# Optimization experiments

Measured on AMD Instinct MI355X. Metric: run time of the kernel, lower is better.

The kernel has to match this reference:

```python
import jax, jax.numpy as jnp
import numpy as np

HEADS = 8

def group_conv1x1(x, w, heads):
    # x: (B, Cin, H, W); w: (Cout, Cin//heads, 1, 1) grouped 1x1 conv, no bias
    B, Cin, H, W = x.shape
    Cout = w.shape[0]
    xg = x.reshape(B, heads, Cin // heads, H * W)
    wg = w[:, :, 0, 0].reshape(heads, Cout // heads, Cin // heads)
    out = jnp.einsum('hoc,bhcl->bhol', wg, xg)
    return out.reshape(B, Cout, H, W)

def sine_pe(d_model, length):
    # standard transformer sin/cos encoding, laid out as (d_model, length)
    pos = jnp.arange(length, dtype=jnp.float32)
    i = jnp.arange(0, d_model, 2, dtype=jnp.float32)
    div = jnp.exp(-(jnp.log(10000.0)) * i / d_model)
    ang = div[:, None] * pos[None, :]            # (d/2, L)
    pe = jnp.zeros((d_model, length), dtype=jnp.float32)
    pe = pe.at[0::2].set(jnp.sin(ang)).at[1::2].set(jnp.cos(ang))
    return pe

def setup_inputs() -> dict:
    key = jax.random.key(0)
    k0, k1, k2, k3 = jax.random.split(key, 4)
    B, Cin, H, W = 16, 256, 32, 32
    Cout, heads = 256, HEADS
    fan_out = Cout  # kaiming_normal fan_out for 1x1 conv = Cout*1*1
    std = np.sqrt(2.0 / fan_out)
    x = jax.random.normal(k0, (B, Cin, H, W), dtype=jnp.float32)
    wq = jax.random.normal(k1, (Cout, Cin // heads, 1, 1), dtype=jnp.float32) * std
    wk = jax.random.normal(k2, (Cout, Cin // heads, 1, 1), dtype=jnp.float32) * std
    wv = jax.random.normal(k3, (Cout, Cin // heads, 1, 1), dtype=jnp.float32) * std
    return {"x": x, "wq": wq, "wk": wk, "wv": wv}

def reference(x, wq, wk, wv):
    B, Cin, H, W = x.shape
    Cout = wq.shape[0]
    heads = HEADS
    dh = Cout // heads
    L = H * W

    q = group_conv1x1(x, wq, heads)              # (B, Cout, H, W)
    k = group_conv1x1(x, wk, heads)
    v = group_conv1x1(x, wv, heads)

    # sine positional encoding added to keys over flattened spatial positions
    k = k.reshape(B, Cout, L) + sine_pe(Cout, L)[None]

    q = q.reshape(B, heads, dh, L)               # (B, h, dh, L)
    k = k.reshape(B, heads, dh, L)
    v = v.reshape(B, heads, dh, L)

    scores = jnp.einsum('bhdq,bhdk->bhqk', q, k)  # (B, h, L, L) -- no sqrt(d) scaling, as in source
    attn = jax.nn.softmax(scores, axis=-1)
    out = jnp.einsum('bhqk,bhdk->bhdq', attn, v)  # (B, h, dh, L)
    return out.reshape(B, Cout, H, W)
```

## Files before the change

### kernel.cpp

```cpp
#include <hip/hip_runtime.h>

#define LL   1024
#define BHD  128
#define LOG2E 1.44269504088896340736f

typedef unsigned int       uint;
typedef unsigned short     ushort;
typedef unsigned long long ull;

typedef __attribute__((ext_vector_type(8)))  __bf16          bf16x8;
typedef __attribute__((ext_vector_type(8)))  unsigned short  u16x8;
typedef __attribute__((ext_vector_type(4)))  unsigned short  u16x4;
typedef __attribute__((ext_vector_type(4)))  uint            ui32x4;
typedef __attribute__((ext_vector_type(4)))  float           f32x4;
typedef __attribute__((ext_vector_type(16))) float           f32x16;

static __device__ __forceinline__ ushort f2bf(float f){
  union {float f; uint u;} v; v.f = f;
  uint u = v.u + 0x7fffu + ((v.u >> 16) & 1u);
  return (ushort)(u >> 16);
}
static __device__ __forceinline__ uint pack2(float a, float b){
  return (uint)f2bf(a) | ((uint)f2bf(b) << 16);
}
static __device__ __forceinline__ uint packtrunc(float a, float b){
  union {float f; uint u;} x, y; x.f = a; y.f = b;
  return __builtin_amdgcn_perm(y.u, x.u, 0x07060302u);
}
static __device__ __forceinline__ bf16x8 ld_frag(const ushort* p){
  u16x8 t = *(const u16x8*)p;
  return __builtin_bit_cast(bf16x8, t);
}
static __device__ __forceinline__ bf16x8 ld_frag64(const ushort* p){
  u16x4 a = *(const u16x4*)p;
  u16x4 b = *(const u16x4*)(p + 4);
  u16x8 t;
  t[0]=a[0]; t[1]=a[1]; t[2]=a[2]; t[3]=a[3];
  t[4]=b[0]; t[5]=b[1]; t[6]=b[2]; t[7]=b[3];
  return __builtin_bit_cast(bf16x8, t);
}

static __device__ __forceinline__ bool sniff_is_bf16(const uint* xw, int tid, int* cnt){
  uint w = xw[tid & 255];
  uint e = (w >> 7) & 0xFFu;
  bool hit = (e >= 118u) && (e <= 132u);
  ull b = __ballot(hit);
  if ((tid & 63) == 0) cnt[tid >> 6] = __popcll(b);
  __syncthreads();
  bool r = (cnt[0] + cnt[1] + cnt[2] + cnt[3]) > 128;
  __syncthreads();
  return r;
}

__global__ __launch_bounds__(256) void qkv_kernel(
    const void* __restrict__ xr,
    const void* __restrict__ wqr,
    const void* __restrict__ wkr,
    const void* __restrict__ wvr,
    ushort* __restrict__ Qt, ushort* __restrict__ Kt, ushort* __restrict__ Vt)
{
  const int bh   = blockIdx.x;
  const int lt   = blockIdx.y;
  const int tid  = threadIdx.x;
  const int wave = tid >> 6;
  const int lane = tid & 63;
  const int l16  = lane & 15;
  const int quad = lane >> 4;
  const int lbase = lt * 128;

  __shared__ int cnt[4];
  __shared__ __align__(16) uint xsd[128][20];

  const bool is_bf = sniff_is_bf16((const uint*)xr, tid, cnt);

  {
    const int cp = tid & 15, lg = tid >> 4;
    const size_t rb = (size_t)(bh*32 + 2*cp)*LL + lbase + lg*8;
    uint dw[8];
    if (is_bf){
      u16x8 e = *(const u16x8*)((const ushort*)xr + rb);
      u16x8 o = *(const u16x8*)((const ushort*)xr + rb + LL);
      #pragma unroll
      for (int j = 0; j < 8; ++j) dw[j] = (uint)e[j] | ((uint)o[j] << 16);
    } else {
      const float* xf = (const float*)xr;
      float4 e0 = *(const float4*)(xf + rb);
      float4 e1 = *(const float4*)(xf + rb + 4);
      float4 o0 = *(const float4*)(xf + rb + LL);
      float4 o1 = *(const float4*)(xf + rb + LL + 4);
      dw[0]=pack2(e0.x,o0.x); dw[1]=pack2(e0.y,o0.y);
      dw[2]=pack2(e0.z,o0.z); dw[3]=pack2(e0.w,o0.w);
      dw[4]=pack2(e1.x,o1.x); dw[5]=pack2(e1.y,o1.y);
      dw[6]=pack2(e1.z,o1.z); dw[7]=pack2(e1.w,o1.w);
    }
    #pragma unroll
    for (int j = 0; j < 8; ++j) xsd[lg*8 + j][cp] = dw[j];
  }
  __syncthreads();

  const void* wsrc[3] = {wqr, wkr, wvr};
  bf16x8 bw[3][2];
  #pragma unroll
  for (int p = 0; p < 3; ++p)
    #pragma unroll
    for (int nh = 0; nh < 2; ++nh){
      const int row = (bh & 7)*32 + nh*16 + l16;
      if (is_bf){
        bw[p][nh] = ld_frag((const ushort*)wsrc[p] + (size_t)row*32 + quad*8);
      } else {
        const float* wf = (const float*)wsrc[p] + (size_t)row*32 + quad*8;
        float4 f0 = *(const float4*)wf, f1 = *(const float4*)(wf + 4);
        u16x8 t;
        t[0]=f2bf(f0.x); t[1]=f2bf(f0.y); t[2]=f2bf(f0.z); t[3]=f2bf(f0.w);
        t[4]=f2bf(f1.x); t[5]=f2bf(f1.y); t[6]=f2bf(f1.z); t[7]=f2bf(f1.w);
        bw[p][nh] = __builtin_bit_cast(bf16x8, t);
      }
    }

  bf16x8 ax[2];
  #pragma unroll
  for (int mt = 0; mt < 2; ++mt)
    ax[mt] = __builtin_bit_cast(bf16x8,
               *(const ui32x4*)&xsd[wave*32 + mt*16 + l16][quad*4]);

  const f32x4 z = {0.f,0.f,0.f,0.f};
  f32x4 dq[2][2], dk[2][2], dv[2][2];
  #pragma unroll
  for (int mt = 0; mt < 2; ++mt)
    #pragma unroll
    for (int nh = 0; nh < 2; ++nh){
      dq[mt][nh] = __builtin_amdgcn_mfma_f32_16x16x32_bf16(ax[mt], bw[0][nh], z, 0,0,0);
      dk[mt][nh] = __builtin_amdgcn_mfma_f32_16x16x32_bf16(ax[mt], bw[1][nh], z, 0,0,0);
      dv[nh][mt] = __builtin_amdgcn_mfma_f32_16x16x32_bf16(bw[2][nh], ax[mt], z, 0,0,0);
    }

  #pragma unroll
  for (int mt = 0; mt < 2; ++mt)
    #pragma unroll
    for (int nh = 0; nh < 2; ++nh)
      #pragma unroll
      for (int r = 0; r < 4; ++r){
        const int l = lbase + wave*32 + mt*16 + quad*4 + r;
        const int d = nh*16 + l16;
        Qt[((size_t)bh*LL + l)*32 + d] = f2bf(dq[mt][nh][r]);
      }
  #pragma unroll
  for (int mt = 0; mt < 2; ++mt)
    #pragma unroll
    for (int nh = 0; nh < 2; ++nh){
      const int d = nh*16 + l16;
      const int c = (bh & 7)*32 + d;
      const float freq = __expf(-0.03597789207f * (float)(c & ~1));
      #pragma unroll
      for (int r = 0; r < 4; ++r){
        const int l = lbase + wave*32 + mt*16 + quad*4 + r;
        const float ang = freq * (float)l;
        const float pe  = (c & 1) ? __cosf(ang) : __sinf(ang);
        Kt[((size_t)bh*LL + l)*32 + d] = f2bf((dk[mt][nh][r] + pe) * LOG2E);
      }
    }
  #pragma unroll
  for (int dh = 0; dh < 2; ++dh)
    #pragma unroll
    for (int mt = 0; mt < 2; ++mt)
      #pragma unroll
      for (int r = 0; r < 4; ++r){
        const int d = dh*16 + quad*4 + r;
        const int l = lbase + wave*32 + mt*16 + l16;
        Vt[((size_t)(bh*32 + d))*LL + l] = f2bf(dv[dh][mt][r]);
      }
}

__global__ __launch_bounds__(256, 4) void attn_kernel(
    const void*   __restrict__ xr,
    const ushort* __restrict__ Qt,
    const ushort* __restrict__ Kt,
    const ushort* __restrict__ Vt,
    void* __restrict__ out)
{
  const int bh  = blockIdx.x;
  const int qt  = blockIdx.y;
  const int tid = threadIdx.x;
  const int wave = tid >> 6;
  const int lane = tid & 63;
  const int q32  = lane & 31;
  const int h    = lane >> 5;

  __shared__ int cnt[4];
  __shared__ __align__(16) ushort Ks[128][40];
  __shared__ __align__(16) ushort Vs[32][132];

  const bool is_bf = sniff_is_bf16((const uint*)xr, tid, cnt);

  const int qg = qt*128 + wave*32 + q32;
  const ushort* qrow = Qt + ((size_t)bh*LL + qg)*32;
  bf16x8 bq0 = ld_frag(qrow + h*8);
  bf16x8 bq1 = ld_frag(qrow + 16 + h*8);

  bf16x8 ones;
  { u16x8 t;
    #pragma unroll
    for (int j = 0; j < 8; ++j) t[j] = 0x3F80u;
    ones = __builtin_bit_cast(bf16x8, t); }

  const int skey = tid >> 1, shalf = tid & 1;
  const int rotw = (skey >> 2) & 3;
  const ushort* kg0 = Kt + ((size_t)(bh*LL + skey))*32 + (2*shalf)*8;
  ushort* kw0 = &Ks[skey][((2*shalf     + rotw) & 3)*8];
  ushort* kw1 = &Ks[skey][((2*shalf + 1 + rotw) & 3)*8];
  const int sd = tid >> 3, sg = tid & 7;
  const ushort* vgp = Vt + ((size_t)(bh*32 + sd))*LL + sg*16;
  ushort* vw = &Vs[sd][sg*16];

  const int rot = (q32 >> 2) & 3;
  const ushort* ka0 = &Ks[q32][((h + rot) & 3)*8];
  const ushort* ka1 = &Ks[q32][((2 + h + rot) & 3)*8];
  const ushort* vr  = &Vs[q32][h*8];

  f32x16 O = {};
  f32x16 R = {};

  u16x8 k0 = *(const u16x8*)kg0;
  u16x8 k1 = *(const u16x8*)(kg0 + 8);
  u16x8 v0 = *(const u16x8*)vgp;
  u16x8 v1 = *(const u16x8*)(vgp + 8);

  for (int it = 0; it < 8; ++it){
    __syncthreads();
    *(ui32x4*)kw0 = __builtin_bit_cast(ui32x4, k0);
    *(ui32x4*)kw1 = __builtin_bit_cast(ui32x4, k1);
    {
      u16x4 a, b;
      a[0]=v0[0]; a[1]=v0[1]; a[2]=v0[2]; a[3]=v0[3];
      b[0]=v0[4]; b[1]=v0[5]; b[2]=v0[6]; b[3]=v0[7];
      *(u16x4*)vw = a; *(u16x4*)(vw + 4) = b;
      a[0]=v1[0]; a[1]=v1[1]; a[2]=v1[2]; a[3]=v1[3];
      b[0]=v1[4]; b[1]=v1[5]; b[2]=v1[6]; b[3]=v1[7];
      *(u16x4*)(vw + 8) = a; *(u16x4*)(vw + 12) = b;
    }
    __syncthreads();
    if (it < 7){
      const int ko = (it + 1)*128;
      k0 = *(const u16x8*)(kg0 + (size_t)ko*32);
      k1 = *(const u16x8*)(kg0 + (size_t)ko*32 + 8);
      v0 = *(const u16x8*)(vgp + ko);
      v1 = *(const u16x8*)(vgp + ko + 8);
    }

    #pragma unroll
    for (int u = 0; u < 2; ++u){
      f32x16 st[2];
      #pragma unroll
      for (int tt = 0; tt < 2; ++tt){
        const int t = 2*u + tt;
        bf16x8 a0 = ld_frag(ka0 + t*32*40);
        bf16x8 a1 = ld_frag(ka1 + t*32*40);
        f32x16 zz = {};
        f32x16 s  = __builtin_amdgcn_mfma_f32_32x32x16_bf16(a0, bq0, zz, 0,0,0);
        st[tt]    = __builtin_amdgcn_mfma_f32_32x32x16_bf16(a1, bq1, s,  0,0,0);
      }

      uint pr[2][8];
      #pragma unroll
      for (int tt = 0; tt < 2; ++tt)
        #pragma unroll
        for (int zi = 0; zi < 8; ++zi){
          float p0 = __builtin_amdgcn_exp2f(st[tt][2*zi]);
          float p1 = __builtin_amdgcn_exp2f(st[tt][2*zi+1]);
          pr[tt][zi] = packtrunc(p0, p1);
        }

      #pragma unroll
      for (int c = 0; c < 4; ++c){
        const int tt = c >> 1, g0 = 4*(c & 1);
        uint s0 = h ? pr[tt][g0+0] : pr[tt][g0+2];
        uint s1 = h ? pr[tt][g0+1] : pr[tt][g0+3];
        uint r0 = (uint)__shfl_xor((int)s0, 32);
        uint r1 = (uint)__shfl_xor((int)s1, 32);
        ui32x4 pb;
        pb[0] = h ? r0 : pr[tt][g0+0];
        pb[1] = h ? r1 : pr[tt][g0+1];
        pb[2] = h ? pr[tt][g0+2] : r0;
        pb[3] = h ? pr[tt][g0+3] : r1;
        bf16x8 pf = __builtin_bit_cast(bf16x8, pb);
        bf16x8 va = ld_frag64(vr + (u*4 + c)*16);
        O = __builtin_amdgcn_mfma_f32_32x32x16_bf16(va,   pf, O, 0,0,0);
        R = __builtin_amdgcn_mfma_f32_32x32x16_bf16(ones, pf, R, 0,0,0);
      }
    }
  }

  const float inv = 1.f / R[0];

  #pragma unroll
  for (int reg = 0; reg < 16; ++reg){
    const int d = (reg & 3) + 8*(reg >> 2) + 4*h;
    const float v = O[reg] * inv;
    const size_t off = ((size_t)(bh*32 + d))*LL + qg;
    if (is_bf) ((ushort*)out)[off] = f2bf(v);
    else       ((float*)out)[off]  = v;
  }
}

extern "C" void kernel_launch(void* const* d_in, const int* in_sizes, int n_in,
                              void* d_out, int out_size, void* d_ws, size_t ws_size,
                              hipStream_t stream) {
  const void* x  = d_in[0];
  const void* wq = d_in[1];
  const void* wk = d_in[2];
  const void* wv = d_in[3];

  ushort* Qt = (ushort*)d_ws;
  ushort* Kt = Qt + (size_t)BHD * LL * 32;
  ushort* Vt = Kt + (size_t)BHD * LL * 32;

  qkv_kernel <<<dim3(BHD, 8), 256, 0, stream>>>(x, wq, wk, wv, Qt, Kt, Vt);
  attn_kernel<<<dim3(BHD, 8), 256, 0, stream>>>(x, Qt, Kt, Vt, d_out);
}
```

Baseline: 114.2 us.

## Double-buffer K/V shared tiles to drop one barrier per iteration

The attention kernel now keeps two shared-memory buffers each for the K and V tiles. The next tile's global loads are written into the alternate buffer after compute, so each iteration needs one barrier instead of two. The V row stride is padded from 132 to 136 so rows are 16-byte aligned, which lets V fragments be read with 128-bit loads instead of two 64-bit loads. This doubles LDS use per block, which could lower occupancy at 4 blocks per CU, and the padding may change LDS bank-conflict behaviour.

```diff
diff --git a/kernel.cpp b/kernel.cpp
--- a/kernel.cpp
+++ b/kernel.cpp
@@ -29,14 +29,6 @@
 }
 static __device__ __forceinline__ bf16x8 ld_frag(const ushort* p){
   u16x8 t = *(const u16x8*)p;
-  return __builtin_bit_cast(bf16x8, t);
-}
-static __device__ __forceinline__ bf16x8 ld_frag64(const ushort* p){
-  u16x4 a = *(const u16x4*)p;
-  u16x4 b = *(const u16x4*)(p + 4);
-  u16x8 t;
-  t[0]=a[0]; t[1]=a[1]; t[2]=a[2]; t[3]=a[3];
-  t[4]=b[0]; t[5]=b[1]; t[6]=b[2]; t[7]=b[3];
   return __builtin_bit_cast(bf16x8, t);
 }
 
@@ -187,8 +179,8 @@
   const int h    = lane >> 5;
 
   __shared__ int cnt[4];
-  __shared__ __align__(16) ushort Ks[128][40];
-  __shared__ __align__(16) ushort Vs[32][132];
+  __shared__ __align__(16) ushort Ks[2][128][40];
+  __shared__ __align__(16) ushort Vs[2][32][136];
 
   const bool is_bf = sniff_is_bf16((const uint*)xr, tid, cnt);
 
@@ -206,16 +198,14 @@
   const int skey = tid >> 1, shalf = tid & 1;
   const int rotw = (skey >> 2) & 3;
   const ushort* kg0 = Kt + ((size_t)(bh*LL + skey))*32 + (2*shalf)*8;
-  ushort* kw0 = &Ks[skey][((2*shalf     + rotw) & 3)*8];
-  ushort* kw1 = &Ks[skey][((2*shalf + 1 + rotw) & 3)*8];
+  const int kwo0 = ((2*shalf     + rotw) & 3)*8;
+  const int kwo1 = ((2*shalf + 1 + rotw) & 3)*8;
   const int sd = tid >> 3, sg = tid & 7;
   const ushort* vgp = Vt + ((size_t)(bh*32 + sd))*LL + sg*16;
-  ushort* vw = &Vs[sd][sg*16];
 
   const int rot = (q32 >> 2) & 3;
-  const ushort* ka0 = &Ks[q32][((h + rot) & 3)*8];
-  const ushort* ka1 = &Ks[q32][((2 + h + rot) & 3)*8];
-  const ushort* vr  = &Vs[q32][h*8];
+  const int ko0 = ((h + rot) & 3)*8;
+  const int ko1 = ((2 + h + rot) & 3)*8;
 
   f32x16 O = {};
   f32x16 R = {};
@@ -224,21 +214,15 @@
   u16x8 k1 = *(const u16x8*)(kg0 + 8);
   u16x8 v0 = *(const u16x8*)vgp;
   u16x8 v1 = *(const u16x8*)(vgp + 8);
+  *(ui32x4*)&Ks[0][skey][kwo0] = __builtin_bit_cast(ui32x4, k0);
+  *(ui32x4*)&Ks[0][skey][kwo1] = __builtin_bit_cast(ui32x4, k1);
+  *(ui32x4*)&Vs[0][sd][sg*16]     = __builtin_bit_cast(ui32x4, v0);
+  *(ui32x4*)&Vs[0][sd][sg*16 + 8] = __builtin_bit_cast(ui32x4, v1);
+  __syncthreads();
 
   for (int it = 0; it < 8; ++it){
-    __syncthreads();
-    *(ui32x4*)kw0 = __builtin_bit_cast(ui32x4, k0);
-    *(ui32x4*)kw1 = __builtin_bit_cast(ui32x4, k1);
-    {
-      u16x4 a, b;
-      a[0]=v0[0]; a[1]=v0[1]; a[2]=v0[2]; a[3]=v0[3];
-      b[0]=v0[4]; b[1]=v0[5]; b[2]=v0[6]; b[3]=v0[7];
-      *(u16x4*)vw = a; *(u16x4*)(vw + 4) = b;
-      a[0]=v1[0]; a[1]=v1[1]; a[2]=v1[2]; a[3]=v1[3];
-      b[0]=v1[4]; b[1]=v1[5]; b[2]=v1[6]; b[3]=v1[7];
-      *(u16x4*)(vw + 8) = a; *(u16x4*)(vw + 12) = b;
-    }
-    __syncthreads();
+    const int cur = it & 1;
+
     if (it < 7){
       const int ko = (it + 1)*128;
       k0 = *(const u16x8*)(kg0 + (size_t)ko*32);
@@ -253,8 +237,8 @@
       #pragma unroll
       for (int tt = 0; tt < 2; ++tt){
         const int t = 2*u + tt;
-        bf16x8 a0 = ld_frag(ka0 + t*32*40);
-        bf16x8 a1 = ld_frag(ka1 + t*32*40);
+        bf16x8 a0 = ld_frag(&Ks[cur][t*32 + q32][ko0]);
+        bf16x8 a1 = ld_frag(&Ks[cur][t*32 + q32][ko1]);
         f32x16 zz = {};
         f32x16 s  = __builtin_amdgcn_mfma_f32_32x32x16_bf16(a0, bq0, zz, 0,0,0);
         st[tt]    = __builtin_amdgcn_mfma_f32_32x32x16_bf16(a1, bq1, s,  0,0,0);
@@ -283,11 +267,20 @@
         pb[2] = h ? pr[tt][g0+2] : r0;
         pb[3] = h ? pr[tt][g0+3] : r1;
         bf16x8 pf = __builtin_bit_cast(bf16x8, pb);
-        bf16x8 va = ld_frag64(vr + (u*4 + c)*16);
+        bf16x8 va = ld_frag(&Vs[cur][q32][(u*4 + c)*16 + h*8]);
         O = __builtin_amdgcn_mfma_f32_32x32x16_bf16(va,   pf, O, 0,0,0);
         R = __builtin_amdgcn_mfma_f32_32x32x16_bf16(ones, pf, R, 0,0,0);
       }
     }
+
+    if (it < 7){
+      const int nb = cur ^ 1;
+      *(ui32x4*)&Ks[nb][skey][kwo0] = __builtin_bit_cast(ui32x4, k0);
+      *(ui32x4*)&Ks[nb][skey][kwo1] = __builtin_bit_cast(ui32x4, k1);
+      *(ui32x4*)&Vs[nb][sd][sg*16]     = __builtin_bit_cast(ui32x4, v0);
+      *(ui32x4*)&Vs[nb][sd][sg*16 + 8] = __builtin_bit_cast(ui32x4, v1);
+    }
+    __syncthreads();
   }
 
   const float inv = 1.f / R[0];
```

New measurement: 114.5 us. About the same (+0.3%).
